# Kernel tuning notes

Measured on AMD Instinct MI355X. Metric: run time of the kernel, lower is better.

Reference implementation:

```python
import jax, jax.numpy as jnp
import numpy as np

B, H, V, T = 32768, 1024, 9, 20
EOS = 8

def setup_inputs() -> dict:
    key = jax.random.key(0)
    ks = jax.random.split(key, 10)
    s_fc = 1.0 / np.sqrt(784)
    s_ih = 1.0 / np.sqrt(V)
    s_hh = 1.0 / np.sqrt(H)
    u = jax.random.uniform(ks[9], (T, B, V), jnp.float32, 1e-10, 1.0)
    return {
        "x": jax.random.normal(ks[0], (B, 784), jnp.float32),
        "tau": jnp.float32(1.0),
        "fc_w": jax.random.normal(ks[1], (H, 784), jnp.float32) * s_fc,
        "w_ih": jax.random.normal(ks[2], (3 * H, V), jnp.float32) * s_ih,
        "w_hh": jax.random.normal(ks[3], (3 * H, H), jnp.float32) * s_hh,
        "b_ih": jax.random.normal(ks[4], (3 * H,), jnp.float32) * s_hh,
        "b_hh": jax.random.normal(ks[5], (3 * H,), jnp.float32) * s_hh,
        "proj_w": jax.random.normal(ks[6], (V, H), jnp.float32) * s_hh,
        "proj_b": jax.random.normal(ks[7], (V,), jnp.float32) * s_hh,
        # standard Gumbel(0,1) noise, precomputed for all T steps
        "gumbel": -jnp.log(-jnp.log(u)),
    }


def reference(x, tau, fc_w, w_ih, w_hh, b_ih, b_hh, proj_w, proj_b, gumbel):
    # context = gelu(fc(x)); dropout is identity (eval mode)
    h0 = jax.nn.gelu(x @ fc_w.T, approximate=False)  # [B, H]
    b = x.shape[0]
    tok0 = jnp.zeros((b, V), x.dtype).at[:, 0].set(1.0)  # BOS one-hot

    def step(carry, g):
        h, tok, finished, lengths, t = carry
        gi = tok @ w_ih.T + b_ih            # [B, 3H]
        gh = h @ w_hh.T + b_hh              # [B, 3H]
        i_r, i_z, i_n = jnp.split(gi, 3, axis=-1)
        h_r, h_z, h_n = jnp.split(gh, 3, axis=-1)
        r = jax.nn.sigmoid(i_r + h_r)
        z = jax.nn.sigmoid(i_z + h_z)
        n = jnp.tanh(i_n + r * h_n)
        h_new = (1.0 - z) * n + z * h
        logits = h_new @ proj_w.T + proj_b  # [B, V]
        y_soft = jax.nn.softmax((logits + g) / tau, axis=-1)
        idx = jnp.argmax(y_soft, axis=-1)
        y_hard = jax.nn.one_hot(idx, V, dtype=y_soft.dtype)
        y = y_hard + y_soft - jax.lax.stop_gradient(y_soft)  # straight-through
        newly = (idx == EOS) & (~finished)
        lengths = jnp.where(newly, t + 1, lengths)
        finished = finished | newly
        return (h_new, y, finished, lengths, t + 1), y

    carry0 = (h0, tok0,
              jnp.zeros((b,), jnp.bool_),
              jnp.full((b,), T, jnp.int32),
              jnp.int32(0))
    (_, _, _, lengths, _), toks = jax.lax.scan(step, carry0, gumbel)
    message = jnp.transpose(toks, (1, 0, 2))  # [B, T, V]
    return message, lengths
```

## Files before the change

### kernel.cpp

```cpp
#include <hip/hip_runtime.h>
#include <math.h>

#define Bsz 32768
#define Hd  1024
#define Vn  9
#define Tn  20
#define EOSv 8
#define KFC 784
#define PLANE 33554432ull

typedef float f4 __attribute__((ext_vector_type(4)));
typedef float f32x16 __attribute__((ext_vector_type(16)));
typedef _Float16 h8 __attribute__((ext_vector_type(8)));
typedef unsigned short us4 __attribute__((ext_vector_type(4)));
typedef unsigned short us8v __attribute__((ext_vector_type(8)));

__device__ __forceinline__ unsigned short f16_rne(float x) {
    _Float16 h = (_Float16)x;
    return __builtin_bit_cast(unsigned short, h);
}
__device__ __forceinline__ float f16_val(unsigned short u) {
    return (float)__builtin_bit_cast(_Float16, u);
}
__device__ __forceinline__ void split2h(float x, unsigned short& p0, unsigned short& p1) {
    p0 = f16_rne(x);
    float r = x - f16_val(p0);
    p1 = f16_rne(r);
}
__device__ __forceinline__ int slotr(int r) { return r ^ ((r >> 3) & 3); }

__global__ __launch_bounds__(256) void k_init(int* __restrict__ st,
                                              float* __restrict__ lenf) {
    int i = blockIdx.x * 256 + threadIdx.x;
    if (i < Bsz) { st[i] = 0; lenf[i] = (float)Tn; }
}

__global__ __launch_bounds__(256) void k_prep(const float* __restrict__ wih,
                                              const float* __restrict__ bih,
                                              float* __restrict__ giTab) {
    int i = blockIdx.x * 256 + threadIdx.x;
    int tk = i / 3072, n = i - tk * 3072;
    giTab[i] = wih[(size_t)n * Vn + tk] + bih[n];
}

__global__ __launch_bounds__(256) void k_prepB(const float* __restrict__ whh,
                                               unsigned short* __restrict__ wp) {
    int g = blockIdx.x * 256 + threadIdx.x;
    int lane = g & 63, u = g >> 6;
    int p = u & 1, kc = (u >> 1) & 63, ct = u >> 7;
    int col = ct * 32 + (lane & 31);
    int k = kc * 16 + (lane >> 5) * 8;
    const float* src = whh + (size_t)col * Hd + k;
    unsigned short v[8];
    #pragma unroll
    for (int i = 0; i < 8; ++i) {
        unsigned short s0, s1; split2h(src[i], s0, s1);
        v[i] = (p == 0) ? s0 : s1;
    }
    unsigned short* dst = wp + (size_t)u * 512 + lane * 8;
    us4 w0; w0[0]=v[0]; w0[1]=v[1]; w0[2]=v[2]; w0[3]=v[3];
    us4 w1; w1[0]=v[4]; w1[1]=v[5]; w1[2]=v[6]; w1[3]=v[7];
    *(us4*)dst = w0;
    *(us4*)(dst + 4) = w1;
}

__global__ __launch_bounds__(256) void k_fcP(const float* __restrict__ x,
                                             const float* __restrict__ fcw,
                                             float* __restrict__ h0,
                                             unsigned short* __restrict__ hp) {
    __shared__ float As[16][68];
    __shared__ float Ws[16][68];
    const int tid = threadIdx.x;
    const int tx = tid & 15, ty = tid >> 4;
    const int m0 = blockIdx.x * 64, n0 = blockIdx.y * 64;
    const int lrow = tid >> 2, lkc = (tid & 3) << 2;
    float acc[4][4] = {};
    for (int k0 = 0; k0 < KFC; k0 += 16) {
        f4 a = *(const f4*)(x   + (size_t)(m0 + lrow) * KFC + k0 + lkc);
        f4 w = *(const f4*)(fcw + (size_t)(n0 + lrow) * KFC + k0 + lkc);
        #pragma unroll
        for (int q = 0; q < 4; ++q) { As[lkc + q][lrow] = a[q]; Ws[lkc + q][lrow] = w[q]; }
        __syncthreads();
        #pragma unroll
        for (int kk = 0; kk < 16; ++kk) {
            f4 av = *(const f4*)&As[kk][ty * 4];
            f4 wv = *(const f4*)&Ws[kk][tx * 4];
            #pragma unroll
            for (int i = 0; i < 4; ++i)
                #pragma unroll
                for (int j = 0; j < 4; ++j)
                    acc[i][j] = fmaf(av[i], wv[j], acc[i][j]);
        }
        __syncthreads();
    }
    #pragma unroll
    for (int i = 0; i < 4; ++i) {
        int b = m0 + ty * 4 + i;
        int cb = n0 + tx * 4;
        f4 hv;
        us4 q0, q1;
        #pragma unroll
        for (int j = 0; j < 4; ++j) {
            float v = acc[i][j];
            float gl = 0.5f * v * (1.0f + erff(v * 0.70710678118654752f));
            hv[j] = gl;
            unsigned short s0, s1; split2h(gl, s0, s1);
            q0[j] = s0; q1[j] = s1;
        }
        *(f4*)&h0[(size_t)b * Hd + cb] = hv;
        *(us4*)&hp[0 * PLANE + (size_t)b * Hd + cb] = q0;
        *(us4*)&hp[1 * PLANE + (size_t)b * Hd + cb] = q1;
    }
}

__global__ __launch_bounds__(256, 2) void k_step(
        const unsigned short* __restrict__ hp, float* __restrict__ h,
        const unsigned short* __restrict__ wp, const float* __restrict__ bhh,
        const float* __restrict__ giTab, const int* __restrict__ st) {
    __shared__ unsigned short Asm[2][2 * 4 * 128 * 8];
    const int tid = threadIdx.x;
    const int lane = tid & 63, wid = tid >> 6;
    const int wm = wid >> 1, wn = wid & 1;
    const int l31 = lane & 31, lh = lane >> 5;

    const int w = blockIdx.x;
    const int cg = (w & 7) * 2 + ((w >> 3) & 1);
    const int rb = w >> 4;
    const int m_blk = rb * 128;
    const int c0 = cg * 64;

    f32x16 acc[2][3];
    #pragma unroll
    for (int mt = 0; mt < 2; ++mt)
        #pragma unroll
        for (int g = 0; g < 3; ++g)
            #pragma unroll
            for (int e = 0; e < 16; ++e) acc[mt][g][e] = 0.0f;

    const int ar = tid >> 1;
    const int kqw = (tid & 1) << 1;
    const int wslot = slotr(ar);
    int rslot[2];
    #pragma unroll
    for (int mt = 0; mt < 2; ++mt) rslot[mt] = slotr(wm * 64 + mt * 32 + l31);

    const unsigned short* bg[3];
    #pragma unroll
    for (int g = 0; g < 3; ++g) {
        int ct = g * 32 + cg * 2 + wn;
        bg[g] = wp + (size_t)ct * 64 * 2 * 512 + (size_t)lane * 8;
    }

    us8v pa[2][2];
    auto load_a = [&](int s) {
        const size_t base = (size_t)(m_blk + ar) * Hd + (s << 5) + (kqw << 3);
        pa[0][0] = *(const us8v*)&hp[0 * PLANE + base];
        pa[0][1] = *(const us8v*)&hp[0 * PLANE + base + 8];
        pa[1][0] = *(const us8v*)&hp[1 * PLANE + base];
        pa[1][1] = *(const us8v*)&hp[1 * PLANE + base + 8];
    };
    auto write_a = [&](int bufi) {
        #pragma unroll
        for (int p = 0; p < 2; ++p)
            #pragma unroll
            for (int half = 0; half < 2; ++half)
                *(us8v*)&Asm[bufi][((p * 4 + kqw + half) * 128 + wslot) * 8] = pa[p][half];
    };

    load_a(0);
    write_a(0);
    load_a(1);
    __syncthreads();

    for (int s = 0; s < 32; ++s) {
        const int bi = s & 1;
        if (s < 31) write_a(bi ^ 1);
        if (s < 30) load_a(s + 2);
        #pragma unroll
        for (int kc = 0; kc < 2; ++kc) {
            h8 af[2][2];
            #pragma unroll
            for (int mt = 0; mt < 2; ++mt)
                #pragma unroll
                for (int p = 0; p < 2; ++p)
                    af[mt][p] = *(const h8*)&Asm[bi][((p * 4 + kc * 2 + lh) * 128 + rslot[mt]) * 8];
            #pragma unroll
            for (int g = 0; g < 3; ++g) {
                const unsigned short* bp = bg[g] + ((size_t)(s * 2 + kc) * 2) * 512;
                h8 b0 = *(const h8*)(bp);
                h8 b1 = *(const h8*)(bp + 512);
                #pragma unroll
                for (int mt = 0; mt < 2; ++mt) {
                    f32x16 c = acc[mt][g];
                    c = __builtin_amdgcn_mfma_f32_32x32x16_f16(af[mt][0], b1, c, 0, 0, 0);
                    c = __builtin_amdgcn_mfma_f32_32x32x16_f16(af[mt][1], b0, c, 0, 0, 0);
                    c = __builtin_amdgcn_mfma_f32_32x32x16_f16(af[mt][0], b0, c, 0, 0, 0);
                    acc[mt][g] = c;
                }
            }
        }
        __syncthreads();
    }

    const int col = c0 + wn * 32 + l31;
    const float bhr = bhh[col], bhz = bhh[Hd + col], bhn = bhh[2 * Hd + col];
    #pragma unroll
    for (int mt = 0; mt < 2; ++mt) {
        #pragma unroll
        for (int reg = 0; reg < 16; ++reg) {
            const int row = m_blk + wm * 64 + mt * 32 + 4 * lh + (reg & 3) + 8 * (reg >> 2);
            const int tk = st[row] & 15;
            const float* gi = giTab + tk * 3072;
            float rr = 1.0f / (1.0f + expf(-(gi[col] + acc[mt][0][reg] + bhr)));
            float zz = 1.0f / (1.0f + expf(-(gi[Hd + col] + acc[mt][1][reg] + bhz)));
            float nn = tanhf(gi[2 * Hd + col] + rr * (acc[mt][2][reg] + bhn));
            const size_t off = (size_t)row * Hd + col;
            float hold = h[off];
            h[off] = (1.0f - zz) * nn + zz * hold;
        }
    }
}

__global__ __launch_bounds__(256) void k_projP(const float* __restrict__ hnew,
        unsigned short* __restrict__ hp,
        const float* __restrict__ pw, const float* __restrict__ pb,
        const float* __restrict__ gum, const float* __restrict__ tau,
        float* __restrict__ msg, float* __restrict__ lenf,
        int* __restrict__ st, int t) {
    const int lane = threadIdx.x & 63;
    const int wv = threadIdx.x >> 6;
    const int b = blockIdx.x * 4 + wv;
    const float* hr = hnew + (size_t)b * Hd;
    float s[Vn] = {};
    float vals[16];
    #pragma unroll
    for (int c0 = 0; c0 < 16; c0 += 4) {
        f4 hv = *(const f4*)(hr + lane * 16 + c0);
        #pragma unroll
        for (int q = 0; q < 4; ++q) vals[c0 + q] = hv[q];
        #pragma unroll
        for (int v = 0; v < Vn; ++v) {
            f4 pv = *(const f4*)(pw + (size_t)v * Hd + lane * 16 + c0);
            #pragma unroll
            for (int q = 0; q < 4; ++q) s[v] = fmaf(hv[q], pv[q], s[v]);
        }
    }
    us8v o0[2], o1[2];
    #pragma unroll
    for (int hh = 0; hh < 2; ++hh)
        #pragma unroll
        for (int e = 0; e < 8; ++e) {
            unsigned short q0, q1;
            split2h(vals[hh * 8 + e], q0, q1);
            o0[hh][e] = q0; o1[hh][e] = q1;
        }
    size_t base = (size_t)b * Hd + lane * 16;
    #pragma unroll
    for (int hh = 0; hh < 2; ++hh) {
        *(us8v*)&hp[0 * PLANE + base + hh * 8] = o0[hh];
        *(us8v*)&hp[1 * PLANE + base + hh * 8] = o1[hh];
    }
    #pragma unroll
    for (int v = 0; v < Vn; ++v)
        #pragma unroll
        for (int off = 32; off > 0; off >>= 1)
            s[v] += __shfl_xor(s[v], off, 64);
    if (lane == 0) {
        const float tv = tau[0];
        float zv[Vn];
        #pragma unroll
        for (int v = 0; v < Vn; ++v)
            zv[v] = (s[v] + pb[v] + gum[(size_t)b * Vn + v]) / tv;
        int idx = 0; float m = zv[0];
        #pragma unroll
        for (int v = 1; v < Vn; ++v)
            if (zv[v] > m) { m = zv[v]; idx = v; }
        float* orow = msg + ((size_t)b * Tn + t) * Vn;
        #pragma unroll
        for (int v = 0; v < Vn; ++v) orow[v] = (v == idx) ? 1.0f : 0.0f;
        const int old = st[b];
        const int fn = old >> 4;
        st[b] = idx | (((fn != 0) || (idx == EOSv)) ? 16 : 0);
        if (idx == EOSv && fn == 0) lenf[b] = (float)(t + 1);
    }
}

extern "C" void kernel_launch(void* const* d_in, const int* in_sizes, int n_in,
                              void* d_out, int out_size, void* d_ws, size_t ws_size,
                              hipStream_t stream) {
    const float* x   = (const float*)d_in[0];
    const float* tau = (const float*)d_in[1];
    const float* fcw = (const float*)d_in[2];
    const float* wih = (const float*)d_in[3];
    const float* whh = (const float*)d_in[4];
    const float* bih = (const float*)d_in[5];
    const float* bhh = (const float*)d_in[6];
    const float* pw  = (const float*)d_in[7];
    const float* pb  = (const float*)d_in[8];
    const float* gum = (const float*)d_in[9];

    float* msg  = (float*)d_out;
    float* lenf = msg + (size_t)Bsz * Tn * Vn;

    char* ws = (char*)d_ws;
    float*          h     = (float*)ws;
    unsigned short* hp    = (unsigned short*)(ws + 134217728ull);
    unsigned short* wpb   = (unsigned short*)(ws + 268435456ull);
    float*          giTab = (float*)(ws + 281018368ull);
    int*            st    = (int*)  (ws + 281128960ull);

    k_init<<<Bsz / 256, 256, 0, stream>>>(st, lenf);
    k_prep<<<108, 256, 0, stream>>>(wih, bih, giTab);
    k_prepB<<<3072, 256, 0, stream>>>(whh, wpb);
    k_fcP<<<dim3(Bsz / 64, Hd / 64), 256, 0, stream>>>(x, fcw, h, hp);
    for (int t = 0; t < Tn; ++t) {
        k_step<<<4096, 256, 0, stream>>>(hp, h, wpb, bhh, giTab, st);
        k_projP<<<Bsz / 4, 256, 0, stream>>>(h, hp, pw, pb,
                                             gum + (size_t)t * Bsz * Vn,
                                             tau, msg, lenf, st, t);
    }
}
```

Before: 18.15 ms.

## Software-pipeline B-fragment loads and halve A-tile K step in GRU step GEMM

Restructures the k_step main loop to use a K-step of 16 instead of 32, halving the shared-memory A buffer, and prefetches the weight (B) fragments into registers one step ahead with an explicit double-buffered, two-stage unrolled loop. The goal is to hide global-load latency of the weight fragments behind MFMA work and to reduce LDS footprint. In exchange there are twice as many barriers per K sweep and more live registers for the B prefetch buffers, which may affect occupancy.

```diff
diff --git a/kernel.cpp b/kernel.cpp
--- a/kernel.cpp
+++ b/kernel.cpp
@@ -117,7 +117,7 @@
         const unsigned short* __restrict__ hp, float* __restrict__ h,
         const unsigned short* __restrict__ wp, const float* __restrict__ bhh,
         const float* __restrict__ giTab, const int* __restrict__ st) {
-    __shared__ unsigned short Asm[2][2 * 4 * 128 * 8];
+    __shared__ unsigned short Asm[2][2 * 2 * 128 * 8];
     const int tid = threadIdx.x;
     const int lane = tid & 63, wid = tid >> 6;
     const int wm = wid >> 1, wn = wid & 1;
@@ -138,7 +138,7 @@
             for (int e = 0; e < 16; ++e) acc[mt][g][e] = 0.0f;
 
     const int ar = tid >> 1;
-    const int kqw = (tid & 1) << 1;
+    const int kh = tid & 1;
     const int wslot = slotr(ar);
     int rslot[2];
     #pragma unroll
@@ -151,54 +151,67 @@
         bg[g] = wp + (size_t)ct * 64 * 2 * 512 + (size_t)lane * 8;
     }
 
-    us8v pa[2][2];
+    us8v pa[2];
     auto load_a = [&](int s) {
-        const size_t base = (size_t)(m_blk + ar) * Hd + (s << 5) + (kqw << 3);
-        pa[0][0] = *(const us8v*)&hp[0 * PLANE + base];
-        pa[0][1] = *(const us8v*)&hp[0 * PLANE + base + 8];
-        pa[1][0] = *(const us8v*)&hp[1 * PLANE + base];
-        pa[1][1] = *(const us8v*)&hp[1 * PLANE + base + 8];
+        const size_t base = (size_t)(m_blk + ar) * Hd + (s << 4) + (kh << 3);
+        pa[0] = *(const us8v*)&hp[0 * PLANE + base];
+        pa[1] = *(const us8v*)&hp[1 * PLANE + base];
     };
-    auto write_a = [&](int bufi) {
-        #pragma unroll
-        for (int p = 0; p < 2; ++p)
-            #pragma unroll
-            for (int half = 0; half < 2; ++half)
-                *(us8v*)&Asm[bufi][((p * 4 + kqw + half) * 128 + wslot) * 8] = pa[p][half];
+    auto write_a = [&](unsigned short* buf) {
+        *(us8v*)&buf[((0 * 2 + kh) * 128 + wslot) * 8] = pa[0];
+        *(us8v*)&buf[((1 * 2 + kh) * 128 + wslot) * 8] = pa[1];
     };
-
+    auto load_b = [&](int s, h8* bb) {
+        #pragma unroll
+        for (int g = 0; g < 3; ++g) {
+            const unsigned short* bp = bg[g] + ((size_t)s * 2) * 512;
+            bb[g * 2 + 0] = *(const h8*)(bp);
+            bb[g * 2 + 1] = *(const h8*)(bp + 512);
+        }
+    };
+    auto compute = [&](const unsigned short* Abuf, const h8* bb) {
+        h8 af[2][2];
+        #pragma unroll
+        for (int mt = 0; mt < 2; ++mt)
+            #pragma unroll
+            for (int p = 0; p < 2; ++p)
+                af[mt][p] = *(const h8*)&Abuf[((p * 2 + lh) * 128 + rslot[mt]) * 8];
+        #pragma unroll
+        for (int g = 0; g < 3; ++g) {
+            h8 b0 = bb[g * 2 + 0];
+            h8 b1 = bb[g * 2 + 1];
+            #pragma unroll
+            for (int mt = 0; mt < 2; ++mt) {
+                f32x16 c = acc[mt][g];
+                c = __builtin_amdgcn_mfma_f32_32x32x16_f16(af[mt][0], b1, c, 0, 0, 0);
+                c = __builtin_amdgcn_mfma_f32_32x32x16_f16(af[mt][1], b0, c, 0, 0, 0);
+                c = __builtin_amdgcn_mfma_f32_32x32x16_f16(af[mt][0], b0, c, 0, 0, 0);
+                acc[mt][g] = c;
+            }
+        }
+    };
+
+    h8 B0[6], B1[6];
+
+    load_b(0, B0);
     load_a(0);
-    write_a(0);
+    write_a(Asm[0]);
     load_a(1);
     __syncthreads();
 
-    for (int s = 0; s < 32; ++s) {
-        const int bi = s & 1;
-        if (s < 31) write_a(bi ^ 1);
-        if (s < 30) load_a(s + 2);
-        #pragma unroll
-        for (int kc = 0; kc < 2; ++kc) {
-            h8 af[2][2];
-            #pragma unroll
-            for (int mt = 0; mt < 2; ++mt)
-                #pragma unroll
-                for (int p = 0; p < 2; ++p)
-                    af[mt][p] = *(const h8*)&Asm[bi][((p * 4 + kc * 2 + lh) * 128 + rslot[mt]) * 8];
-            #pragma unroll
-            for (int g = 0; g < 3; ++g) {
-                const unsigned short* bp = bg[g] + ((size_t)(s * 2 + kc) * 2) * 512;
-                h8 b0 = *(const h8*)(bp);
-                h8 b1 = *(const h8*)(bp + 512);
-                #pragma unroll
-                for (int mt = 0; mt < 2; ++mt) {
-                    f32x16 c = acc[mt][g];
-                    c = __builtin_amdgcn_mfma_f32_32x32x16_f16(af[mt][0], b1, c, 0, 0, 0);
-                    c = __builtin_amdgcn_mfma_f32_32x32x16_f16(af[mt][1], b0, c, 0, 0, 0);
-                    c = __builtin_amdgcn_mfma_f32_32x32x16_f16(af[mt][0], b0, c, 0, 0, 0);
-                    acc[mt][g] = c;
-                }
-            }
-        }
+    for (int s2 = 0; s2 < 32; ++s2) {
+        const int s = s2 * 2;
+        load_b(s + 1, B1);
+        write_a(Asm[1]);
+        if (s < 62) load_a(s + 2);
+        compute(Asm[0], B0);
+        __syncthreads();
+        if (s + 2 < 64) {
+            load_b(s + 2, B0);
+            write_a(Asm[0]);
+            if (s + 3 < 64) load_a(s + 3);
+        }
+        compute(Asm[1], B1);
         __syncthreads();
     }
 
```

Measured after the change: 16.89 ms. 1.08x faster.

## Store hidden state pre-swizzled in MFMA fragment layout and drop LDS staging

Applied to the files above, without the earlier changes.

The fp16 hi/lo split of the hidden state is now written by the fc and projection kernels directly in the per-lane MFMA operand layout, matching the pre-packed weight layout. The GRU step kernel then loads A and B fragments straight from global memory into registers with a two-stage register double buffer, removing the shared-memory tile, its writes and the barriers. This trades LDS reuse for more global/L2 traffic, since the four waves no longer share A tiles through shared memory, and raises register pressure from the doubled fragment buffers.

```diff
diff --git a/kernel.cpp b/kernel.cpp
--- a/kernel.cpp
+++ b/kernel.cpp
@@ -7,7 +7,6 @@
 #define Tn  20
 #define EOSv 8
 #define KFC 784
-#define PLANE 33554432ull
 
 typedef float f4 __attribute__((ext_vector_type(4)));
 typedef float f32x16 __attribute__((ext_vector_type(16)));
@@ -27,7 +26,6 @@
     float r = x - f16_val(p0);
     p1 = f16_rne(r);
 }
-__device__ __forceinline__ int slotr(int r) { return r ^ ((r >> 3) & 3); }
 
 __global__ __launch_bounds__(256) void k_init(int* __restrict__ st,
                                               float* __restrict__ lenf) {
@@ -67,7 +65,7 @@
 __global__ __launch_bounds__(256) void k_fcP(const float* __restrict__ x,
                                              const float* __restrict__ fcw,
                                              float* __restrict__ h0,
-                                             unsigned short* __restrict__ hp) {
+                                             unsigned short* __restrict__ ap) {
     __shared__ float As[16][68];
     __shared__ float Ws[16][68];
     const int tid = threadIdx.x;
@@ -95,8 +93,8 @@
     }
     #pragma unroll
     for (int i = 0; i < 4; ++i) {
-        int b = m0 + ty * 4 + i;
-        int cb = n0 + tx * 4;
+        const int row = m0 + ty * 4 + i;
+        const int cb = n0 + tx * 4;
         f4 hv;
         us4 q0, q1;
         #pragma unroll
@@ -107,17 +105,19 @@
             unsigned short s0, s1; split2h(gl, s0, s1);
             q0[j] = s0; q1[j] = s1;
         }
-        *(f4*)&h0[(size_t)b * Hd + cb] = hv;
-        *(us4*)&hp[0 * PLANE + (size_t)b * Hd + cb] = q0;
-        *(us4*)&hp[1 * PLANE + (size_t)b * Hd + cb] = q1;
+        *(f4*)&h0[(size_t)row * Hd + cb] = hv;
+        const size_t ub = ((size_t)(row >> 5) * 64 + (cb >> 4)) * 2;
+        const int slot = (row & 31) + ((cb >> 3) & 1) * 32;
+        const int eo = (tx & 1) * 4;
+        *(us4*)&ap[(ub + 0) * 512 + slot * 8 + eo] = q0;
+        *(us4*)&ap[(ub + 1) * 512 + slot * 8 + eo] = q1;
     }
 }
 
 __global__ __launch_bounds__(256, 2) void k_step(
-        const unsigned short* __restrict__ hp, float* __restrict__ h,
+        const unsigned short* __restrict__ ap, float* __restrict__ h,
         const unsigned short* __restrict__ wp, const float* __restrict__ bhh,
         const float* __restrict__ giTab, const int* __restrict__ st) {
-    __shared__ unsigned short Asm[2][2 * 4 * 128 * 8];
     const int tid = threadIdx.x;
     const int lane = tid & 63, wid = tid >> 6;
     const int wm = wid >> 1, wn = wid & 1;
@@ -137,69 +137,55 @@
             #pragma unroll
             for (int e = 0; e < 16; ++e) acc[mt][g][e] = 0.0f;
 
-    const int ar = tid >> 1;
-    const int kqw = (tid & 1) << 1;
-    const int wslot = slotr(ar);
-    int rslot[2];
-    #pragma unroll
-    for (int mt = 0; mt < 2; ++mt) rslot[mt] = slotr(wm * 64 + mt * 32 + l31);
-
-    const unsigned short* bg[3];
-    #pragma unroll
-    for (int g = 0; g < 3; ++g) {
-        int ct = g * 32 + cg * 2 + wn;
-        bg[g] = wp + (size_t)ct * 64 * 2 * 512 + (size_t)lane * 8;
-    }
-
-    us8v pa[2][2];
-    auto load_a = [&](int s) {
-        const size_t base = (size_t)(m_blk + ar) * Hd + (s << 5) + (kqw << 3);
-        pa[0][0] = *(const us8v*)&hp[0 * PLANE + base];
-        pa[0][1] = *(const us8v*)&hp[0 * PLANE + base + 8];
-        pa[1][0] = *(const us8v*)&hp[1 * PLANE + base];
-        pa[1][1] = *(const us8v*)&hp[1 * PLANE + base + 8];
+    const unsigned short* ab[2][2];
+    #pragma unroll
+    for (int mt = 0; mt < 2; ++mt)
+        #pragma unroll
+        for (int p = 0; p < 2; ++p)
+            ab[mt][p] = ap + ((size_t)(rb * 4 + wm * 2 + mt) * 64 * 2 + p) * 512 + lane * 8;
+    const unsigned short* bb[3][2];
+    #pragma unroll
+    for (int g = 0; g < 3; ++g)
+        #pragma unroll
+        for (int p = 0; p < 2; ++p)
+            bb[g][p] = wp + ((size_t)(g * 32 + cg * 2 + wn) * 64 * 2 + p) * 512 + lane * 8;
+
+    h8 A0[2][2], A1[2][2], B0[3][2], B1[3][2];
+
+    auto load = [&](int s, h8 (&A)[2][2], h8 (&B)[3][2]) {
+        const size_t off = (size_t)s * 1024;
+        #pragma unroll
+        for (int mt = 0; mt < 2; ++mt)
+            #pragma unroll
+            for (int p = 0; p < 2; ++p)
+                A[mt][p] = *(const h8*)(ab[mt][p] + off);
+        #pragma unroll
+        for (int g = 0; g < 3; ++g)
+            #pragma unroll
+            for (int p = 0; p < 2; ++p)
+                B[g][p] = *(const h8*)(bb[g][p] + off);
     };
-    auto write_a = [&](int bufi) {
-        #pragma unroll
-        for (int p = 0; p < 2; ++p)
-            #pragma unroll
-            for (int half = 0; half < 2; ++half)
-                *(us8v*)&Asm[bufi][((p * 4 + kqw + half) * 128 + wslot) * 8] = pa[p][half];
-    };
-
-    load_a(0);
-    write_a(0);
-    load_a(1);
-    __syncthreads();
-
-    for (int s = 0; s < 32; ++s) {
-        const int bi = s & 1;
-        if (s < 31) write_a(bi ^ 1);
-        if (s < 30) load_a(s + 2);
-        #pragma unroll
-        for (int kc = 0; kc < 2; ++kc) {
-            h8 af[2][2];
-            #pragma unroll
-            for (int mt = 0; mt < 2; ++mt)
-                #pragma unroll
-                for (int p = 0; p < 2; ++p)
-                    af[mt][p] = *(const h8*)&Asm[bi][((p * 4 + kc * 2 + lh) * 128 + rslot[mt]) * 8];
-            #pragma unroll
-            for (int g = 0; g < 3; ++g) {
-                const unsigned short* bp = bg[g] + ((size_t)(s * 2 + kc) * 2) * 512;
-                h8 b0 = *(const h8*)(bp);
-                h8 b1 = *(const h8*)(bp + 512);
+    auto compute = [&](h8 (&A)[2][2], h8 (&B)[3][2]) {
+        #pragma unroll
+        for (int ps = 0; ps < 3; ++ps)
+            #pragma unroll
+            for (int g = 0; g < 3; ++g)
                 #pragma unroll
                 for (int mt = 0; mt < 2; ++mt) {
-                    f32x16 c = acc[mt][g];
-                    c = __builtin_amdgcn_mfma_f32_32x32x16_f16(af[mt][0], b1, c, 0, 0, 0);
-                    c = __builtin_amdgcn_mfma_f32_32x32x16_f16(af[mt][1], b0, c, 0, 0, 0);
-                    c = __builtin_amdgcn_mfma_f32_32x32x16_f16(af[mt][0], b0, c, 0, 0, 0);
-                    acc[mt][g] = c;
+                    h8 a = (ps == 1) ? A[mt][1] : A[mt][0];
+                    h8 b = (ps == 0) ? B[g][1] : B[g][0];
+                    acc[mt][g] = __builtin_amdgcn_mfma_f32_32x32x16_f16(a, b, acc[mt][g], 0, 0, 0);
                 }
-            }
-        }
-        __syncthreads();
+    };
+
+    load(0, A0, B0);
+    load(1, A1, B1);
+    for (int s2 = 0; s2 < 32; ++s2) {
+        const int s = s2 * 2;
+        compute(A0, B0);
+        if (s + 2 < 64) load(s + 2, A0, B0);
+        compute(A1, B1);
+        if (s + 3 < 64) load(s + 3, A1, B1);
     }
 
     const int col = c0 + wn * 32 + l31;
@@ -222,7 +208,7 @@
 }
 
 __global__ __launch_bounds__(256) void k_projP(const float* __restrict__ hnew,
-        unsigned short* __restrict__ hp,
+        unsigned short* __restrict__ ap,
         const float* __restrict__ pw, const float* __restrict__ pb,
         const float* __restrict__ gum, const float* __restrict__ tau,
         float* __restrict__ msg, float* __restrict__ lenf,
@@ -254,12 +240,12 @@
             split2h(vals[hh * 8 + e], q0, q1);
             o0[hh][e] = q0; o1[hh][e] = q1;
         }
-    size_t base = (size_t)b * Hd + lane * 16;
-    #pragma unroll
-    for (int hh = 0; hh < 2; ++hh) {
-        *(us8v*)&hp[0 * PLANE + base + hh * 8] = o0[hh];
-        *(us8v*)&hp[1 * PLANE + base + hh * 8] = o1[hh];
-    }
+    const size_t ub = ((size_t)(b >> 5) * 64 + lane) * 2;
+    const int sl = (b & 31) * 8;
+    *(us8v*)&ap[(ub + 0) * 512 + sl]       = o0[0];
+    *(us8v*)&ap[(ub + 0) * 512 + sl + 256] = o0[1];
+    *(us8v*)&ap[(ub + 1) * 512 + sl]       = o1[0];
+    *(us8v*)&ap[(ub + 1) * 512 + sl + 256] = o1[1];
     #pragma unroll
     for (int v = 0; v < Vn; ++v)
         #pragma unroll
@@ -304,7 +290,7 @@
 
     char* ws = (char*)d_ws;
     float*          h     = (float*)ws;
-    unsigned short* hp    = (unsigned short*)(ws + 134217728ull);
+    unsigned short* apb   = (unsigned short*)(ws + 134217728ull);
     unsigned short* wpb   = (unsigned short*)(ws + 268435456ull);
     float*          giTab = (float*)(ws + 281018368ull);
     int*            st    = (int*)  (ws + 281128960ull);
@@ -312,10 +298,10 @@
     k_init<<<Bsz / 256, 256, 0, stream>>>(st, lenf);
     k_prep<<<108, 256, 0, stream>>>(wih, bih, giTab);
     k_prepB<<<3072, 256, 0, stream>>>(whh, wpb);
-    k_fcP<<<dim3(Bsz / 64, Hd / 64), 256, 0, stream>>>(x, fcw, h, hp);
+    k_fcP<<<dim3(Bsz / 64, Hd / 64), 256, 0, stream>>>(x, fcw, h, apb);
     for (int t = 0; t < Tn; ++t) {
-        k_step<<<4096, 256, 0, stream>>>(hp, h, wpb, bhh, giTab, st);
-        k_projP<<<Bsz / 4, 256, 0, stream>>>(h, hp, pw, pb,
+        k_step<<<4096, 256, 0, stream>>>(apb, h, wpb, bhh, giTab, st);
+        k_projP<<<Bsz / 4, 256, 0, stream>>>(h, apb, pw, pb,
                                              gum + (size_t)t * Bsz * Vn,
                                              tau, msg, lenf, st, t);
     }
```

Result: no change. 17.98 ms (-1.0%).
